# Performance work log

Measured on AMD Instinct MI355X. Metric: run time of the kernel, lower is better.

## Reference

```python
import jax, jax.numpy as jnp
import numpy as np

B = 64          # batch
C = 80          # num_classes
IN_CH = 300     # word-embedding channel
J = 8192        # JOINT_EMB_SIZE (linear_intermediate)
S = 8           # pooling_stride
OUT = J // S    # out_in_tmp = 1024


def setup_inputs() -> dict:
    key = jax.random.key(0)
    ks = jax.random.split(key, 8)
    w = lambda k, sh: jax.random.normal(k, sh, jnp.float32) * 0.02
    return {
        "feature": jax.random.normal(ks[0], (B, 2048, 14, 14), jnp.float32),
        "inp": jax.random.normal(ks[1], (1, C, IN_CH), jnp.float32),
        "A": jax.random.uniform(ks[2], (C, C), jnp.float32),  # positive co-occurrence adjacency
        "W_gc1": w(ks[3], (IN_CH, 1024)),
        "W_gc2": w(ks[4], (1024, 2048)),
        "W_img": w(ks[5], (J, 2048)),
        "b_img": jnp.zeros((J,), jnp.float32),
        "W_cls": w(ks[6], (J, 2048)),
        "b_cls": jnp.zeros((J,), jnp.float32),
        "W_ml": w(ks[7], (C, C * OUT)),
        "b_ml": jnp.zeros((C,), jnp.float32),
    }


def reference(feature, inp, A, W_gc1, W_gc2, W_img, b_img, W_cls, b_cls, W_ml, b_ml):
    # backbone output -> MaxPool2d(14,14) over a 14x14 map == global spatial max
    feat = feature.max(axis=(2, 3))                       # [B, 2048]

    # gen_adj(A).detach(): D = diag(rowsum(A)^-0.5); adj = D @ A.T @ D
    dinv = jnp.sum(A, axis=1) ** -0.5                     # [C]
    adj = jax.lax.stop_gradient(A.T * dinv[:, None] * dinv[None, :])  # [C, C]

    # two GCN layers on label embeddings
    x = adj @ (inp[0] @ W_gc1)                            # [C, 1024]
    x = jax.nn.leaky_relu(x, 0.2)
    x = adj @ (x @ W_gc2)                                 # [C, 2048]

    # MFB bilinear fusion (vectorized form of the nested batch/class loops;
    # dropout is identity in eval mode)
    img = feat @ W_img.T + b_img                          # [B, J]
    cls = x @ W_cls.T + b_cls                             # [C, J]
    # sum-pool over the stride axis of the elementwise product:
    # iq[b,c,o] = sum_s img[b,o*S+s] * cls[c,o*S+s]
    pooled = jnp.einsum('bos,cos->bco',
                        img.reshape(B, OUT, S),
                        cls.reshape(C, OUT, S))           # [B, C, OUT]
    # torch.cat order over class columns -> c-major flatten, then ML_fc_layer
    out = pooled.reshape(B, C * OUT) @ W_ml.T + b_ml      # [B, C]
    return out
```

## Files before the change

### kernel.cpp

```cpp
#include <hip/hip_runtime.h>
#include <hip/hip_bf16.h>
#include <cstdint>
#include <cstddef>

typedef float  f32x4  __attribute__((ext_vector_type(4)));
typedef __bf16 bf16x8 __attribute__((ext_vector_type(8)));
typedef unsigned short u16x8 __attribute__((ext_vector_type(8)));

__device__ __forceinline__ unsigned short f2bf(float f) {
    unsigned u = __float_as_uint(f);
    u += 0x7FFFu + ((u >> 16) & 1u);
    return (unsigned short)(u >> 16);
}


constexpr size_t OFF_FEATB = 0;
constexpr size_t OFF_X2B   = 262144;
constexpr size_t OFF_XB    = 425984;
constexpr size_t OFF_IMG   = 753664;
constexpr size_t OFF_CLS   = 2850816;
constexpr size_t OFF_G     = 5472256;
constexpr size_t OFF_Y0    = 8093696;


__device__ __forceinline__ void maxpool_role(int vbid, const float* __restrict__ feature,
                                             unsigned short* __restrict__ featb,
                                             float4* tile ) {
    int t = threadIdx.x;
    const float4* src = (const float4*)(feature + (size_t)vbid * 32 * 196);
    #pragma unroll
    for (int pass = 0; pass < 6; ++pass)
        tile[pass * 256 + t] = src[pass * 256 + t];
    if (t < 32) tile[1536 + t] = src[1536 + t];
    __syncthreads();

    int r = t >> 3, q = t & 7;
    const float4* row = tile + r * 49;
    float4 v0 = row[q],      v1 = row[q + 8],  v2 = row[q + 16];
    float4 v3 = row[q + 24], v4 = row[q + 32], v5 = row[q + 40];
    float m0 = fmaxf(fmaxf(v0.x, v0.y), fmaxf(v0.z, v0.w));
    float m1 = fmaxf(fmaxf(v1.x, v1.y), fmaxf(v1.z, v1.w));
    float m2 = fmaxf(fmaxf(v2.x, v2.y), fmaxf(v2.z, v2.w));
    float m3 = fmaxf(fmaxf(v3.x, v3.y), fmaxf(v3.z, v3.w));
    float m4 = fmaxf(fmaxf(v4.x, v4.y), fmaxf(v4.z, v4.w));
    float m5 = fmaxf(fmaxf(v5.x, v5.y), fmaxf(v5.z, v5.w));
    float m = fmaxf(fmaxf(fmaxf(m0, m1), fmaxf(m2, m3)), fmaxf(m4, m5));
    if (q == 0) {
        float4 d = row[48];
        m = fmaxf(m, fmaxf(fmaxf(d.x, d.y), fmaxf(d.z, d.w)));
    }
    #pragma unroll
    for (int off = 1; off < 8; off <<= 1) m = fmaxf(m, __shfl_xor(m, off));
    if (q == 0) featb[vbid * 32 + r] = f2bf(m);
}

__device__ __forceinline__ void y0_role(int idx, const float* __restrict__ inp,
                                        const float* __restrict__ W1,
                                        float* __restrict__ y0g, float4* red) {
    int c = idx >> 2;
    int j = (idx & 3) * 256 + (threadIdx.x & 63) * 4;
    int ks = threadIdx.x >> 6;
    const float* ir = inp + c * 300 + ks * 75;
    const float* wp = W1 + (size_t)(ks * 75) * 1024 + j;
    float4 acc = {0.f, 0.f, 0.f, 0.f};
    for (int k = 0; k < 75; k += 3) {
        float a0 = ir[k], a1 = ir[k + 1], a2 = ir[k + 2];
        float4 w0 = *(const float4*)(wp + (size_t)k * 1024);
        float4 w1 = *(const float4*)(wp + (size_t)(k + 1) * 1024);
        float4 w2 = *(const float4*)(wp + (size_t)(k + 2) * 1024);
        acc.x = fmaf(a0, w0.x, acc.x); acc.y = fmaf(a0, w0.y, acc.y);
        acc.z = fmaf(a0, w0.z, acc.z); acc.w = fmaf(a0, w0.w, acc.w);
        acc.x = fmaf(a1, w1.x, acc.x); acc.y = fmaf(a1, w1.y, acc.y);
        acc.z = fmaf(a1, w1.z, acc.z); acc.w = fmaf(a1, w1.w, acc.w);
        acc.x = fmaf(a2, w2.x, acc.x); acc.y = fmaf(a2, w2.y, acc.y);
        acc.z = fmaf(a2, w2.z, acc.z); acc.w = fmaf(a2, w2.w, acc.w);
    }
    int jq = threadIdx.x & 63;
    red[ks * 64 + jq] = __builtin_bit_cast(float4, acc);
    __syncthreads();
    if (ks == 0) {
        float4 s0 = red[jq], s1 = red[64 + jq], s2 = red[128 + jq], s3 = red[192 + jq];
        float4 s;
        s.x = s0.x + s1.x + s2.x + s3.x;
        s.y = s0.y + s1.y + s2.y + s3.y;
        s.z = s0.z + s1.z + s2.z + s3.z;
        s.w = s0.w + s1.w + s2.w + s3.w;
        *(float4*)(y0g + (size_t)c * 1024 + j) = s;
    }
}

__device__ __forceinline__ void x1x2_role(int idx, const float* __restrict__ y0g,
                                          const float* __restrict__ A,
                                          unsigned short* __restrict__ x2b,
                                          float* smem) {
    float* dinv = smem;
    float* ys   = smem + 80;
    float* xs   = smem + 720;
    int t = threadIdx.x;
    int j = t & 7, slot = t >> 3;
    int j0 = idx * 8;
    int c0 = slot, c1 = slot + 32, c2 = slot + 64;
    bool has3 = (slot < 16);

    if (t < 80) {
        const float4* ar = (const float4*)(A + t * 80);
        float4 s4 = {0.f, 0.f, 0.f, 0.f};
        #pragma unroll
        for (int q = 0; q < 20; q++) {
            float4 v = ar[q];
            s4.x += v.x; s4.y += v.y; s4.z += v.z; s4.w += v.w;
        }
        dinv[t] = 1.0f / sqrtf(s4.x + s4.y + s4.z + s4.w);
    }
    __syncthreads();
    ys[c0 * 8 + j] = dinv[c0] * y0g[(size_t)c0 * 1024 + j0 + j];
    ys[c1 * 8 + j] = dinv[c1] * y0g[(size_t)c1 * 1024 + j0 + j];
    if (has3) ys[c2 * 8 + j] = dinv[c2] * y0g[(size_t)c2 * 1024 + j0 + j];
    __syncthreads();

    float b0 = 0.f, b1 = 0.f, b2 = 0.f;
    #pragma unroll 4
    for (int e = 0; e < 80; e++) {
        float y = ys[e * 8 + j];
        b0 = fmaf(A[e * 80 + c0], y, b0);
        b1 = fmaf(A[e * 80 + c1], y, b1);
        if (has3) b2 = fmaf(A[e * 80 + c2], y, b2);
    }
    b0 *= dinv[c0];
    b1 *= dinv[c1];
    b2 *= has3 ? dinv[c2] : 0.f;
    if (b0 < 0.f) b0 *= 0.2f;
    if (b1 < 0.f) b1 *= 0.2f;
    if (b2 < 0.f) b2 *= 0.2f;
    __syncthreads();
    xs[c0 * 8 + j] = dinv[c0] * b0;
    xs[c1 * 8 + j] = dinv[c1] * b1;
    if (has3) xs[c2 * 8 + j] = dinv[c2] * b2;
    __syncthreads();

    float d0 = 0.f, d1 = 0.f, d2 = 0.f;
    #pragma unroll 4
    for (int e = 0; e < 80; e++) {
        float x = xs[e * 8 + j];
        d0 = fmaf(A[e * 80 + c0], x, d0);
        d1 = fmaf(A[e * 80 + c1], x, d1);
        if (has3) d2 = fmaf(A[e * 80 + c2], x, d2);
    }
    x2b[c0 * 1024 + j0 + j] = f2bf(d0 * dinv[c0]);
    x2b[c1 * 1024 + j0 + j] = f2bf(d1 * dinv[c1]);
    if (has3) x2b[c2 * 1024 + j0 + j] = f2bf(d2 * dinv[c2]);
}

template <int MF>
__device__ __forceinline__ void gemm_block(int bx, const unsigned short* __restrict__ X,
                                           const float* __restrict__ W,
                                           const float* __restrict__ bias,
                                           float* __restrict__ outf,
                                           unsigned short* __restrict__ outb,
                                           int N, int K, float (*red)[64][21]) {
    int tid = threadIdx.x;
    int ks = tid >> 6, lane = tid & 63;
    int n = bx * 16 + (lane & 15);
    int rowa = lane & 15;
    int koff = (lane >> 4) * 8;
    int Kc = K >> 2;
    int k0 = ks * Kc;

    f32x4 acc[MF];
    #pragma unroll
    for (int i = 0; i < MF; i++) acc[i] = (f32x4)(0.f);

    const float* wrow = W + (size_t)n * K;

    #pragma unroll 2
    for (int k = k0; k < k0 + Kc; k += 32) {
        float4 w0 = *(const float4*)(wrow + k + koff);
        float4 w1 = *(const float4*)(wrow + k + koff + 4);
        u16x8 bu;
        bu[0] = f2bf(w0.x); bu[1] = f2bf(w0.y); bu[2] = f2bf(w0.z); bu[3] = f2bf(w0.w);
        bu[4] = f2bf(w1.x); bu[5] = f2bf(w1.y); bu[6] = f2bf(w1.z); bu[7] = f2bf(w1.w);
        bf16x8 bf = __builtin_bit_cast(bf16x8, bu);
        #pragma unroll
        for (int mf = 0; mf < MF; mf++) {
            u16x8 au = *(const u16x8*)(X + (size_t)(mf * 16 + rowa) * K + k + koff);
            acc[mf] = __builtin_amdgcn_mfma_f32_16x16x32_bf16(
                __builtin_bit_cast(bf16x8, au), bf, acc[mf], 0, 0, 0);
        }
    }

    #pragma unroll
    for (int mf = 0; mf < MF; mf++)
        #pragma unroll
        for (int i = 0; i < 4; i++)
            red[ks][lane][mf * 4 + i] = acc[mf][i];
    __syncthreads();

    int lane2 = tid & 63, sg = tid >> 6;
    int n2 = bx * 16 + (lane2 & 15);
    float b = bias ? bias[n2] : 0.f;
    #pragma unroll
    for (int mf = 0; mf < MF; mf++) {
        int slot = mf * 4 + sg;
        float s = red[0][lane2][slot] + red[1][lane2][slot]
                + red[2][lane2][slot] + red[3][lane2][slot] + b;
        int row = mf * 16 + (lane2 >> 4) * 4 + sg;
        size_t o = (size_t)row * N + n2;
        if (outf) outf[o] = s;
        if (outb) outb[o] = f2bf(s);
    }
}

template <int MF>
__device__ __forceinline__ void gemm_block_kn(int bx, const unsigned short* __restrict__ X,
                                              const float* __restrict__ Wkn,
                                              const float* __restrict__ bias,
                                              float* __restrict__ outf,
                                              unsigned short* __restrict__ outb,
                                              int N, int K, float (*red)[64][21]) {
    int tid = threadIdx.x;
    int ks = tid >> 6, lane = tid & 63;
    int n = bx * 16 + (lane & 15);
    int rowa = lane & 15;
    int koff = (lane >> 4) * 8;
    int Kc = K >> 2;
    int k0 = ks * Kc;

    f32x4 acc[MF];
    #pragma unroll
    for (int i = 0; i < MF; i++) acc[i] = (f32x4)(0.f);

    #pragma unroll 2
    for (int k = k0; k < k0 + Kc; k += 32) {
        float w[8];
        #pragma unroll
        for (int i = 0; i < 8; i++) w[i] = Wkn[(size_t)(k + koff + i) * N + n];
        u16x8 bu;
        #pragma unroll
        for (int i = 0; i < 8; i++) bu[i] = f2bf(w[i]);
        bf16x8 bf = __builtin_bit_cast(bf16x8, bu);
        #pragma unroll
        for (int mf = 0; mf < MF; mf++) {
            u16x8 au = *(const u16x8*)(X + (size_t)(mf * 16 + rowa) * K + k + koff);
            acc[mf] = __builtin_amdgcn_mfma_f32_16x16x32_bf16(
                __builtin_bit_cast(bf16x8, au), bf, acc[mf], 0, 0, 0);
        }
    }

    #pragma unroll
    for (int mf = 0; mf < MF; mf++)
        #pragma unroll
        for (int i = 0; i < 4; i++)
            red[ks][lane][mf * 4 + i] = acc[mf][i];
    __syncthreads();

    int lane2 = tid & 63, sg = tid >> 6;
    int n2 = bx * 16 + (lane2 & 15);
    float b = bias ? bias[n2] : 0.f;
    #pragma unroll
    for (int mf = 0; mf < MF; mf++) {
        int slot = mf * 4 + sg;
        float s = red[0][lane2][slot] + red[1][lane2][slot]
                + red[2][lane2][slot] + red[3][lane2][slot] + b;
        int row = mf * 16 + (lane2 >> 4) * 4 + sg;
        size_t o = (size_t)row * N + n2;
        if (outf) outf[o] = s;
        if (outb) outb[o] = f2bf(s);
    }
}


__global__ __launch_bounds__(256, 4) void kA(const float* __restrict__ feature,
                                             unsigned short* __restrict__ featb,
                                             const float* __restrict__ inp,
                                             const float* __restrict__ W1,
                                             float* __restrict__ y0g) {
    __shared__ __align__(16) float smem[6272];
    int b = blockIdx.x;
    if (b < 320) y0_role(b, inp, W1, y0g, (float4*)smem);
    else         maxpool_role(b - 320, feature, featb, (float4*)smem);
}

__global__ __launch_bounds__(256, 4) void kB(const float* __restrict__ y0g,
                                             const float* __restrict__ A,
                                             unsigned short* __restrict__ x2b,
                                             const unsigned short* __restrict__ featb,
                                             const float* __restrict__ W_img,
                                             const float* __restrict__ b_img,
                                             float* __restrict__ img) {
    __shared__ __align__(16) float red[4][64][21];
    int b = blockIdx.x;
    if (b < 128) x1x2_role(b, y0g, A, x2b, (float*)red);
    else         gemm_block<4>(b - 128, featb, W_img, b_img, img, nullptr, 8192, 2048, red);
}

__global__ __launch_bounds__(256, 4) void kC(const unsigned short* __restrict__ x2b,
                                             const float* __restrict__ W_gc2,
                                             unsigned short* __restrict__ xb,
                                             const unsigned short* __restrict__ featb,
                                             const float* __restrict__ W_img,
                                             const float* __restrict__ b_img,
                                             float* __restrict__ img) {
    __shared__ __align__(16) float red[4][64][21];
    int b = blockIdx.x;
    if (b < 128) gemm_block_kn<5>(b, x2b, W_gc2, nullptr, nullptr, xb, 2048, 1024, red);
    else         gemm_block<4>(b - 128 + 384, featb, W_img, b_img, img, nullptr, 8192, 2048, red);
}

__global__ __launch_bounds__(256, 4) void kD(const unsigned short* __restrict__ xb,
                                             const float* __restrict__ W_cls,
                                             const float* __restrict__ b_cls,
                                             float* __restrict__ cls) {
    __shared__ __align__(16) float red[4][64][21];
    gemm_block<5>(blockIdx.x, xb, W_cls, b_cls, cls, nullptr, 8192, 2048, red);
}

__global__ __launch_bounds__(256, 4) void kE(const float* __restrict__ cls,
                                             const float* __restrict__ W_ml,
                                             float* __restrict__ G) {
    __shared__ __align__(16) float smem[8 * 80 * 16];
    float (*wml)[80][16] = (float (*)[80][16])smem;
    int idx = blockIdx.x;
    int o0  = (idx & 63) * 16;
    int c2b = (idx >> 6) * 8;
    int j0  = o0 * 8;
    for (int i = threadIdx.x; i < 8 * 80 * 16; i += 256) {
        int ol = i & 15, c = (i >> 4) % 80, c2 = i / 1280;
        wml[c2][c][ol] = W_ml[(size_t)(c2b + c2) * 81920 + c * 1024 + o0 + ol];
    }
    __syncthreads();
    int jl  = threadIdx.x & 127;
    int c2h = (threadIdx.x >> 7) * 4;
    int ol  = jl >> 3;
    float acc[4] = {0.f, 0.f, 0.f, 0.f};
    for (int c = 0; c < 80; c++) {
        float cv = cls[(size_t)c * 8192 + j0 + jl];
        #pragma unroll
        for (int i = 0; i < 4; i++) acc[i] = fmaf(cv, wml[c2h + i][c][ol], acc[i]);
    }
    #pragma unroll
    for (int i = 0; i < 4; i++) G[(size_t)(c2b + c2h + i) * 8192 + j0 + jl] = acc[i];
}

__global__ __launch_bounds__(256, 2) void kF(const float* __restrict__ img,
                                             const float* __restrict__ G,
                                             const float* __restrict__ b_ml,
                                             float* __restrict__ out) {
    __shared__ float sm[4][8];
    int b = blockIdx.x / 10, cg = blockIdx.x % 10;
    int kc = threadIdx.x >> 6, lane = threadIdx.x & 63;
    const float* ib = img + (size_t)b * 8192 + kc * 2048;
    const float* gb = G + (size_t)(cg * 8) * 8192 + kc * 2048;
    float acc[8] = {0.f, 0.f, 0.f, 0.f, 0.f, 0.f, 0.f, 0.f};
    #pragma unroll
    for (int step = 0; step < 8; step++) {
        int k = step * 256 + lane * 4;
        float4 iv = *(const float4*)(ib + k);
        float4 gv[8];
        #pragma unroll
        for (int i = 0; i < 8; i++) gv[i] = *(const float4*)(gb + (size_t)i * 8192 + k);
        #pragma unroll
        for (int i = 0; i < 8; i++) {
            acc[i] = fmaf(iv.x, gv[i].x, acc[i]);
            acc[i] = fmaf(iv.y, gv[i].y, acc[i]);
            acc[i] = fmaf(iv.z, gv[i].z, acc[i]);
            acc[i] = fmaf(iv.w, gv[i].w, acc[i]);
        }
    }
    #pragma unroll
    for (int i = 0; i < 8; i++) {
        float v = acc[i];
        #pragma unroll
        for (int off = 32; off; off >>= 1) v += __shfl_xor(v, off);
        if (lane == 0) sm[kc][i] = v;
    }
    __syncthreads();
    if (threadIdx.x < 8) {
        int i = threadIdx.x;
        float s = b_ml[cg * 8 + i] + sm[0][i] + sm[1][i] + sm[2][i] + sm[3][i];
        out[(size_t)b * 80 + cg * 8 + i] = s;
    }
}

extern "C" void kernel_launch(void* const* d_in, const int* in_sizes, int n_in,
                              void* d_out, int out_size, void* d_ws, size_t ws_size,
                              hipStream_t stream) {
    (void)in_sizes; (void)n_in; (void)out_size; (void)ws_size;
    const float* feature = (const float*)d_in[0];
    const float* inp     = (const float*)d_in[1];
    const float* A       = (const float*)d_in[2];
    const float* W_gc1   = (const float*)d_in[3];
    const float* W_gc2   = (const float*)d_in[4];
    const float* W_img   = (const float*)d_in[5];
    const float* b_img   = (const float*)d_in[6];
    const float* W_cls   = (const float*)d_in[7];
    const float* b_cls   = (const float*)d_in[8];
    const float* W_ml    = (const float*)d_in[9];
    const float* b_ml    = (const float*)d_in[10];
    float* out = (float*)d_out;
    char*  ws  = (char*)d_ws;

    unsigned short* featb = (unsigned short*)(ws + OFF_FEATB);
    unsigned short* x2b   = (unsigned short*)(ws + OFF_X2B);
    unsigned short* xb    = (unsigned short*)(ws + OFF_XB);
    float* img  = (float*)(ws + OFF_IMG);
    float* cls  = (float*)(ws + OFF_CLS);
    float* G    = (float*)(ws + OFF_G);
    float* y0g  = (float*)(ws + OFF_Y0);

    kA<<<4416, 256, 0, stream>>>(feature, featb, inp, W_gc1, y0g);
    kB<<<512,  256, 0, stream>>>(y0g, A, x2b, featb, W_img, b_img, img);
    kC<<<256,  256, 0, stream>>>(x2b, W_gc2, xb, featb, W_img, b_img, img);
    kD<<<512,  256, 0, stream>>>(xb, W_cls, b_cls, cls);
    kE<<<640,  256, 0, stream>>>(cls, W_ml, G);
    kF<<<640,  256, 0, stream>>>(img, G, b_ml, out);
}
```

Baseline: 132.3 us.

## Stream maxpool loads directly from global with nontemporal loads, fewer blocks

The global max-pool role no longer stages each 32-channel tile through shared memory with a barrier. Each thread now reads its row's float4 chunks straight from global memory using nontemporal loads, and each block covers 8 tiles strided across the grid, so kA launches 832 blocks instead of 4416. Shared memory in kA shrinks to the 4 KB needed by the y0 reduction, which may allow higher occupancy. The trade-offs are uncoalesced per-row strided loads and fewer blocks in flight to hide the latency of the large feature read.

```diff
diff --git a/kernel.cpp b/kernel.cpp
--- a/kernel.cpp
+++ b/kernel.cpp
@@ -23,35 +23,31 @@
 constexpr size_t OFF_Y0    = 8093696;
 
 
-__device__ __forceinline__ void maxpool_role(int vbid, const float* __restrict__ feature,
-                                             unsigned short* __restrict__ featb,
-                                             float4* tile ) {
+__device__ __forceinline__ float max4(f32x4 v) {
+    return fmaxf(fmaxf(v.x, v.y), fmaxf(v.z, v.w));
+}
+
+__device__ __forceinline__ void maxpool_role(int bid, const float* __restrict__ feature,
+                                             unsigned short* __restrict__ featb) {
     int t = threadIdx.x;
-    const float4* src = (const float4*)(feature + (size_t)vbid * 32 * 196);
-    #pragma unroll
-    for (int pass = 0; pass < 6; ++pass)
-        tile[pass * 256 + t] = src[pass * 256 + t];
-    if (t < 32) tile[1536 + t] = src[1536 + t];
-    __syncthreads();
-
     int r = t >> 3, q = t & 7;
-    const float4* row = tile + r * 49;
-    float4 v0 = row[q],      v1 = row[q + 8],  v2 = row[q + 16];
-    float4 v3 = row[q + 24], v4 = row[q + 32], v5 = row[q + 40];
-    float m0 = fmaxf(fmaxf(v0.x, v0.y), fmaxf(v0.z, v0.w));
-    float m1 = fmaxf(fmaxf(v1.x, v1.y), fmaxf(v1.z, v1.w));
-    float m2 = fmaxf(fmaxf(v2.x, v2.y), fmaxf(v2.z, v2.w));
-    float m3 = fmaxf(fmaxf(v3.x, v3.y), fmaxf(v3.z, v3.w));
-    float m4 = fmaxf(fmaxf(v4.x, v4.y), fmaxf(v4.z, v4.w));
-    float m5 = fmaxf(fmaxf(v5.x, v5.y), fmaxf(v5.z, v5.w));
-    float m = fmaxf(fmaxf(fmaxf(m0, m1), fmaxf(m2, m3)), fmaxf(m4, m5));
-    if (q == 0) {
-        float4 d = row[48];
-        m = fmaxf(m, fmaxf(fmaxf(d.x, d.y), fmaxf(d.z, d.w)));
-    }
-    #pragma unroll
-    for (int off = 1; off < 8; off <<= 1) m = fmaxf(m, __shfl_xor(m, off));
-    if (q == 0) featb[vbid * 32 + r] = f2bf(m);
+    #pragma unroll
+    for (int it = 0; it < 8; ++it) {
+        int row = (bid + it * 512) * 32 + r;
+        const f32x4* p = (const f32x4*)(feature + (size_t)row * 196);
+        f32x4 v0 = __builtin_nontemporal_load(p + q);
+        f32x4 v1 = __builtin_nontemporal_load(p + q + 8);
+        f32x4 v2 = __builtin_nontemporal_load(p + q + 16);
+        f32x4 v3 = __builtin_nontemporal_load(p + q + 24);
+        f32x4 v4 = __builtin_nontemporal_load(p + q + 32);
+        f32x4 v5 = __builtin_nontemporal_load(p + q + 40);
+        f32x4 v6 = __builtin_nontemporal_load(p + 48);
+        float m = fmaxf(fmaxf(fmaxf(max4(v0), max4(v1)), fmaxf(max4(v2), max4(v3))),
+                        fmaxf(fmaxf(max4(v4), max4(v5)), max4(v6)));
+        #pragma unroll
+        for (int off = 1; off < 8; off <<= 1) m = fmaxf(m, __shfl_xor(m, off));
+        if (q == 0) featb[row] = f2bf(m);
+    }
 }
 
 __device__ __forceinline__ void y0_role(int idx, const float* __restrict__ inp,
@@ -76,7 +72,7 @@
         acc.z = fmaf(a2, w2.z, acc.z); acc.w = fmaf(a2, w2.w, acc.w);
     }
     int jq = threadIdx.x & 63;
-    red[ks * 64 + jq] = __builtin_bit_cast(float4, acc);
+    red[ks * 64 + jq] = acc;
     __syncthreads();
     if (ks == 0) {
         float4 s0 = red[jq], s1 = red[64 + jq], s2 = red[128 + jq], s3 = red[192 + jq];
@@ -274,10 +270,10 @@
                                              const float* __restrict__ inp,
                                              const float* __restrict__ W1,
                                              float* __restrict__ y0g) {
-    __shared__ __align__(16) float smem[6272];
+    __shared__ __align__(16) float4 red[256];
     int b = blockIdx.x;
-    if (b < 320) y0_role(b, inp, W1, y0g, (float4*)smem);
-    else         maxpool_role(b - 320, feature, featb, (float4*)smem);
+    if (b < 320) y0_role(b, inp, W1, y0g, red);
+    else         maxpool_role(b - 320, feature, featb);
 }
 
 __global__ __launch_bounds__(256, 4) void kB(const float* __restrict__ y0g,
@@ -407,7 +403,7 @@
     float* G    = (float*)(ws + OFF_G);
     float* y0g  = (float*)(ws + OFF_Y0);
 
-    kA<<<4416, 256, 0, stream>>>(feature, featb, inp, W_gc1, y0g);
+    kA<<<832,  256, 0, stream>>>(feature, featb, inp, W_gc1, y0g);
     kB<<<512,  256, 0, stream>>>(y0g, A, x2b, featb, W_img, b_img, img);
     kC<<<256,  256, 0, stream>>>(x2b, W_gc2, xb, featb, W_img, b_img, img);
     kD<<<512,  256, 0, stream>>>(xb, W_cls, b_cls, cls);
```

Result: slower. 137.1 us (+3.6%).
